# Performance work log

Hardware: AMD Instinct MI355X
Metric: run time of the kernel (lower is better)

The kernel has to match this reference:

```python
import jax, jax.numpy as jnp
import numpy as np

NUM_HEADS = 16
DIM = 1024

def setup_inputs() -> dict:
    key = jax.random.key(0)
    ks = jax.random.split(key, 12)
    B, N, T, C = 4, 4096, 77, DIM
    s = 1.0 / np.sqrt(C)
    return {
        "hidden_states": jax.random.normal(ks[0], (B, N, C), jnp.float32),
        "encoder_hidden_states": jax.random.normal(ks[1], (B, T, C), jnp.float32),
        "attention_mask": jnp.zeros((B, N, T), jnp.float32),
        "Wq": jax.random.normal(ks[2], (C, C), jnp.float32) * s,
        "bq": jnp.zeros((C,), jnp.float32),
        "Wk": jax.random.normal(ks[3], (C, C), jnp.float32) * s,
        "bk": jnp.zeros((C,), jnp.float32),
        "Wv": jax.random.normal(ks[4], (C, C), jnp.float32) * s,
        "bv": jnp.zeros((C,), jnp.float32),
        "Wo": jax.random.normal(ks[5], (C, C), jnp.float32) * s,
        "bo": jnp.zeros((C,), jnp.float32),
    }

def reference(hidden_states, encoder_hidden_states, attention_mask,
              Wq, bq, Wk, bk, Wv, bv, Wo, bo):
    B, N, C = hidden_states.shape
    T = encoder_hidden_states.shape[1]
    H = NUM_HEADS
    D = C // H
    # QKV projections (torch Linear: x @ W.T + b)
    q = (hidden_states @ Wq.T + bq).reshape(B, N, H, D).transpose(0, 2, 1, 3)   # bhnd
    k = (encoder_hidden_states @ Wk.T + bk).reshape(B, T, H, D).transpose(0, 2, 1, 3)  # bhtd
    v = (encoder_hidden_states @ Wv.T + bv).reshape(B, T, H, D).transpose(0, 2, 1, 3)  # bhtd
    scale = 1.0 / jnp.sqrt(jnp.asarray(D, q.dtype))
    # scores [B,H,N,T]; additive mask broadcast over heads
    scores = jnp.einsum('bhnd,bhtd->bhnt', q, k) * scale + attention_mask[:, None, :, :]
    attn = jax.nn.softmax(scores, axis=-1)
    out = jnp.einsum('bhnt,bhtd->bhnd', attn, v)
    out = out.transpose(0, 2, 1, 3).reshape(B, N, C)
    return out @ Wo.T + bo
```

## Files before the change

### kernel.cpp

```cpp
#include <hip/hip_runtime.h>
#include <cstdint>

typedef __bf16 bf16x8 __attribute__((ext_vector_type(8)));
typedef float f32x4 __attribute__((ext_vector_type(4)));
typedef unsigned short u16;
typedef unsigned int u32;

__device__ __forceinline__ u16 f2bf(float f) {
    u32 u = __builtin_bit_cast(u32, f);
    u += 0x7fffu + ((u >> 16) & 1u);
    return (u16)(u >> 16);
}

__device__ __forceinline__ void gl_lds16(const u16* g, u16* l) {
    __builtin_amdgcn_global_load_lds(
        (const __attribute__((address_space(1))) void*)g,
        (__attribute__((address_space(3))) void*)l,
        16, 0, 0);
}

__device__ __forceinline__ f32x4 mfma16(bf16x8 a, bf16x8 b, f32x4 c) {
    return __builtin_amdgcn_mfma_f32_16x16x32_bf16(a, b, c, 0, 0, 0);
}

__global__ void cvt_pad(const float* __restrict__ src, u16* __restrict__ dst,
                        int srcn, int totn) {
    int i = (blockIdx.x * 256 + threadIdx.x) * 4;
    if (i >= totn) return;
    float4 v = make_float4(0.f, 0.f, 0.f, 0.f);
    if (i < srcn) v = *(const float4*)&src[i];
    ushort4 o;
    o.x = f2bf(v.x); o.y = f2bf(v.y); o.z = f2bf(v.z); o.w = f2bf(v.w);
    *(ushort4*)&dst[i] = o;
}

struct CvtArgs {
    const float* s[5];
    u16* d[5];
    int srcn[5];
    int totn[5];
};

__global__ void cvt_multi(CvtArgs a) {
    const int seg = blockIdx.y;
    int i = (blockIdx.x * 256 + threadIdx.x) * 4;
    if (i >= a.totn[seg]) return;
    float4 v = make_float4(0.f, 0.f, 0.f, 0.f);
    if (i < a.srcn[seg]) v = *(const float4*)&a.s[seg][i];
    ushort4 o;
    o.x = f2bf(v.x); o.y = f2bf(v.y); o.z = f2bf(v.z); o.w = f2bf(v.w);
    *(ushort4*)&a.d[seg][i] = o;
}

__device__ __forceinline__ void store_out(u16* C, long idx, float v) { C[idx] = f2bf(v); }
__device__ __forceinline__ void store_out(float* C, long idx, float v) { C[idx] = v; }

template <typename OutT>
__global__ __launch_bounds__(512, 2) void gemm8p(
    const u16* __restrict__ A, const u16* __restrict__ W,
    const float* __restrict__ bias, OutT* __restrict__ C,
    int M, int N, int K) {
    __shared__ __align__(16) u16 As[2][256 * 64];
    __shared__ __align__(16) u16 Bs[2][256 * 64];

    const int tid = threadIdx.x;
    const int wid = tid >> 6, l = tid & 63;
    const int wr = wid >> 2, wc = wid & 3;
    const int l15 = l & 15, lg = l >> 4;

    const int lin = blockIdx.y * gridDim.x + blockIdx.x;
    const int cpx = (gridDim.x * gridDim.y) >> 3;
    const int swz = (lin & 7) * cpx + (lin >> 3);
    const long tn = swz % gridDim.x;
    const long tm = swz / gridDim.x;

    const u16* Ab = A + tm * 256 * (long)K;
    const u16* Bb = W + tn * 256 * (long)K;

    const int srow = tid >> 3;
    const int schunk = (tid & 7) ^ (srow & 7);
    const long srcoff = (long)srow * K + schunk * 8;

    const int rxor = l15 & 7;
    const int rdo0 = ((0 * 4 + lg) ^ rxor) * 8;
    const int rdo1 = ((1 * 4 + lg) ^ rxor) * 8;

    const int NT = K >> 6;

#define STAGE_A(bufi, q_, t_)                                                 \
    gl_lds16(Ab + (long)(q_)*64 * K + srcoff + (long)(t_)*64,                 \
             &As[bufi][(q_)*4096 + tid * 8])
#define STAGE_B(bufi, q_, t_)                                                 \
    gl_lds16(Bb + (long)(q_)*64 * K + srcoff + (long)(t_)*64,                 \
             &Bs[bufi][(q_)*4096 + tid * 8])

    f32x4 acc[8][4] = {};

#pragma unroll
    for (int q = 0; q < 4; ++q) { STAGE_A(0, q, 0); STAGE_B(0, q, 0); }
#pragma unroll
    for (int q = 0; q < 4; ++q) STAGE_B(1, q, 1);
    STAGE_A(1, 0, 1); STAGE_A(1, 2, 1);
    asm volatile("s_waitcnt vmcnt(6)" ::: "memory");
    __builtin_amdgcn_sched_barrier(0);
    __builtin_amdgcn_s_barrier();

    const int arow = wr * 128 + l15;
    const int brow = wc * 64 + l15;

    for (int t = 0; t < NT; ++t) {
        const int c = t & 1;
        const u16* __restrict__ Ap = &As[c][0];
        const u16* __restrict__ Bp = &Bs[c][0];
        const bool s1 = (t + 1) < NT;
        const bool s2 = (t + 2) < NT;
        bf16x8 b[4][2];

        {
            bf16x8 a[2][2];
#pragma unroll
            for (int mi = 0; mi < 2; ++mi) {
                a[mi][0] = *(const bf16x8*)&Ap[(arow + mi * 16) * 64 + rdo0];
                a[mi][1] = *(const bf16x8*)&Ap[(arow + mi * 16) * 64 + rdo1];
            }
#pragma unroll
            for (int nf = 0; nf < 4; ++nf) {
                b[nf][0] = *(const bf16x8*)&Bp[(brow + nf * 16) * 64 + rdo0];
                b[nf][1] = *(const bf16x8*)&Bp[(brow + nf * 16) * 64 + rdo1];
            }
            if (s1) STAGE_A(c ^ 1, 1, t + 1);
            __builtin_amdgcn_s_barrier();
            asm volatile("s_waitcnt lgkmcnt(0)" ::: "memory");
            __builtin_amdgcn_sched_barrier(0);
            __builtin_amdgcn_s_setprio(1);
#pragma unroll
            for (int mi = 0; mi < 2; ++mi)
#pragma unroll
                for (int nf = 0; nf < 4; ++nf) {
                    acc[mi][nf] = mfma16(a[mi][0], b[nf][0], acc[mi][nf]);
                    acc[mi][nf] = mfma16(a[mi][1], b[nf][1], acc[mi][nf]);
                }
            __builtin_amdgcn_s_setprio(0);
            __builtin_amdgcn_s_barrier();
        }
        {
            bf16x8 a[2][2];
#pragma unroll
            for (int mi = 0; mi < 2; ++mi) {
                a[mi][0] = *(const bf16x8*)&Ap[(arow + (mi + 2) * 16) * 64 + rdo0];
                a[mi][1] = *(const bf16x8*)&Ap[(arow + (mi + 2) * 16) * 64 + rdo1];
            }
            if (s1) STAGE_A(c ^ 1, 3, t + 1);
            if (s2) { STAGE_B(c, 0, t + 2); STAGE_B(c, 1, t + 2); }
            __builtin_amdgcn_s_barrier();
            asm volatile("s_waitcnt lgkmcnt(0)" ::: "memory");
            __builtin_amdgcn_sched_barrier(0);
            __builtin_amdgcn_s_setprio(1);
#pragma unroll
            for (int mi = 0; mi < 2; ++mi)
#pragma unroll
                for (int nf = 0; nf < 4; ++nf) {
                    acc[mi + 2][nf] = mfma16(a[mi][0], b[nf][0], acc[mi + 2][nf]);
                    acc[mi + 2][nf] = mfma16(a[mi][1], b[nf][1], acc[mi + 2][nf]);
                }
            __builtin_amdgcn_s_setprio(0);
            __builtin_amdgcn_s_barrier();
        }
        {
            bf16x8 a[2][2];
#pragma unroll
            for (int mi = 0; mi < 2; ++mi) {
                a[mi][0] = *(const bf16x8*)&Ap[(arow + (mi + 4) * 16) * 64 + rdo0];
                a[mi][1] = *(const bf16x8*)&Ap[(arow + (mi + 4) * 16) * 64 + rdo1];
            }
            if (s2) { STAGE_B(c, 2, t + 2); STAGE_B(c, 3, t + 2); STAGE_A(c, 0, t + 2); }
            __builtin_amdgcn_s_barrier();
            asm volatile("s_waitcnt lgkmcnt(0)" ::: "memory");
            __builtin_amdgcn_sched_barrier(0);
            __builtin_amdgcn_s_setprio(1);
#pragma unroll
            for (int mi = 0; mi < 2; ++mi)
#pragma unroll
                for (int nf = 0; nf < 4; ++nf) {
                    acc[mi + 4][nf] = mfma16(a[mi][0], b[nf][0], acc[mi + 4][nf]);
                    acc[mi + 4][nf] = mfma16(a[mi][1], b[nf][1], acc[mi + 4][nf]);
                }
            __builtin_amdgcn_s_setprio(0);
            __builtin_amdgcn_s_barrier();
        }
        {
            bf16x8 a[2][2];
#pragma unroll
            for (int mi = 0; mi < 2; ++mi) {
                a[mi][0] = *(const bf16x8*)&Ap[(arow + (mi + 6) * 16) * 64 + rdo0];
                a[mi][1] = *(const bf16x8*)&Ap[(arow + (mi + 6) * 16) * 64 + rdo1];
            }
            if (s2) STAGE_A(c, 2, t + 2);
            __builtin_amdgcn_s_barrier();
            asm volatile("s_waitcnt lgkmcnt(0)" ::: "memory");
            __builtin_amdgcn_sched_barrier(0);
            __builtin_amdgcn_s_setprio(1);
#pragma unroll
            for (int mi = 0; mi < 2; ++mi)
#pragma unroll
                for (int nf = 0; nf < 4; ++nf) {
                    acc[mi + 6][nf] = mfma16(a[mi][0], b[nf][0], acc[mi + 6][nf]);
                    acc[mi + 6][nf] = mfma16(a[mi][1], b[nf][1], acc[mi + 6][nf]);
                }
            __builtin_amdgcn_s_setprio(0);
            if (s2)
                asm volatile("s_waitcnt vmcnt(6)" ::: "memory");
            else
                asm volatile("s_waitcnt vmcnt(0)" ::: "memory");
            __builtin_amdgcn_sched_barrier(0);
            __builtin_amdgcn_s_barrier();
        }
    }
#undef STAGE_A
#undef STAGE_B

    const long row0 = tm * 256 + wr * 128;
    const long col0 = tn * 256 + wc * 64;
    float bv[4];
#pragma unroll
    for (int nf = 0; nf < 4; ++nf) bv[nf] = bias[col0 + nf * 16 + l15];
#pragma unroll
    for (int mf = 0; mf < 8; ++mf)
#pragma unroll
        for (int nf = 0; nf < 4; ++nf)
#pragma unroll
            for (int r = 0; r < 4; ++r) {
                const long row = row0 + mf * 16 + lg * 4 + r;
                const long col = col0 + nf * 16 + l15;
                store_out(C, row * N + col, acc[mf][nf][r] + bv[nf]);
            }
}

__device__ __forceinline__ void gemm128_body(
    const u16* __restrict__ A, const u16* __restrict__ W,
    const float* __restrict__ bias, u16* __restrict__ C,
    int N, int K) {
    __shared__ u16 As[128 * 64];
    __shared__ u16 Bs[128 * 64];
    const int tid = threadIdx.x;
    const int w = tid >> 6, l = tid & 63;
    const int wr = w >> 1, wc = w & 1;
    const int l15 = l & 15, lg = l >> 4;
    const long tm = blockIdx.y, tn = blockIdx.x;
    const u16* Ab = A + tm * 128 * (long)K;
    const u16* Bb = W + tn * 128 * (long)K;

    f32x4 acc[4][4] = {};

    for (int k0 = 0; k0 < K; k0 += 64) {
#pragma unroll
        for (int t = 0; t < 4; ++t) {
            int i = t * 256 + tid;
            int row = i >> 3, cc = i & 7;
            gl_lds16(Ab + (long)row * K + k0 + cc * 8, &As[i * 8]);
            gl_lds16(Bb + (long)row * K + k0 + cc * 8, &Bs[i * 8]);
        }
        __syncthreads();
#pragma unroll
        for (int kk = 0; kk < 64; kk += 32) {
            bf16x8 a[4], b[4];
#pragma unroll
            for (int m = 0; m < 4; ++m)
                a[m] = *(const bf16x8*)&As[(wr * 64 + m * 16 + l15) * 64 + kk + lg * 8];
#pragma unroll
            for (int n = 0; n < 4; ++n)
                b[n] = *(const bf16x8*)&Bs[(wc * 64 + n * 16 + l15) * 64 + kk + lg * 8];
#pragma unroll
            for (int m = 0; m < 4; ++m)
#pragma unroll
                for (int n = 0; n < 4; ++n)
                    acc[m][n] = mfma16(a[m], b[n], acc[m][n]);
        }
        __syncthreads();
    }

    const long row0 = tm * 128 + wr * 64;
    const long col0 = tn * 128 + wc * 64;
#pragma unroll
    for (int m = 0; m < 4; ++m)
#pragma unroll
        for (int n = 0; n < 4; ++n)
#pragma unroll
            for (int r = 0; r < 4; ++r) {
                const long row = row0 + m * 16 + lg * 4 + r;
                const long col = col0 + n * 16 + l15;
                C[row * N + col] = f2bf(acc[m][n][r] + bias[col]);
            }
}

__global__ __launch_bounds__(256) void gemm_kv(
    const u16* __restrict__ A,
    const u16* __restrict__ Wk, const float* __restrict__ bk, u16* __restrict__ Ko,
    const u16* __restrict__ Wv, const float* __restrict__ bv, u16* __restrict__ Vo,
    int N, int K) {
    const bool isv = blockIdx.z != 0;
    gemm128_body(A, isv ? Wv : Wk, isv ? bv : bk, isv ? Vo : Ko, N, K);
}

__global__ __launch_bounds__(256) void attn_fused(
    const u16* __restrict__ Q,
    const u16* __restrict__ Kb,
    const u16* __restrict__ Vb,
    const float* __restrict__ mask,
    u16* __restrict__ Ao) {
    __shared__ u16 Ks[96 * 64];
    __shared__ u16 Vt[64 * 96];
    __shared__ u16 Ps[128 * 96];

    const int b = blockIdx.z, h = blockIdx.y, nt = blockIdx.x;
    const int tid = threadIdx.x;
    const int w = tid >> 6, l = tid & 63;
    const int l15 = l & 15, lg = l >> 4;

    for (int c = tid; c < 768; c += 256) {
        const int t = c >> 3, dc = c & 7;
        union { uint4 u; u16 s[8]; } kv, vv;
        kv.u = make_uint4(0, 0, 0, 0);
        vv.u = make_uint4(0, 0, 0, 0);
        if (t < 77) {
            const long base = ((long)(b * 77 + t)) * 1024 + h * 64 + dc * 8;
            kv.u = *(const uint4*)&Kb[base];
            vv.u = *(const uint4*)&Vb[base];
        }
        *(uint4*)&Ks[t * 64 + dc * 8] = kv.u;
#pragma unroll
        for (int j = 0; j < 8; ++j) Vt[(dc * 8 + j) * 96 + t] = vv.s[j];
    }
    __syncthreads();

    f32x4 acc[2][6] = {};
    const long qrow0 = (long)b * 4096 + nt * 128 + w * 32;
#pragma unroll
    for (int kk = 0; kk < 64; kk += 32) {
        bf16x8 a[2], kf[6];
#pragma unroll
        for (int m = 0; m < 2; ++m)
            a[m] = *(const bf16x8*)&Q[(qrow0 + m * 16 + l15) * 1024 + h * 64 + kk + lg * 8];
#pragma unroll
        for (int n = 0; n < 6; ++n)
            kf[n] = *(const bf16x8*)&Ks[(n * 16 + l15) * 64 + kk + lg * 8];
#pragma unroll
        for (int m = 0; m < 2; ++m)
#pragma unroll
            for (int n = 0; n < 6; ++n)
                acc[m][n] = mfma16(a[m], kf[n], acc[m][n]);
    }

    const float* mbase = mask + ((long)b * 4096 + nt * 128 + w * 32) * 77;
#pragma unroll
    for (int m = 0; m < 2; ++m) {
#pragma unroll
        for (int r = 0; r < 4; ++r) {
            const int row = m * 16 + lg * 4 + r;
            float vals[6];
            float rmax = -3e38f;
#pragma unroll
            for (int n = 0; n < 6; ++n) {
                const int col = n * 16 + l15;
                float v = -3e38f;
                if (col < 77) v = acc[m][n][r] * 0.125f + mbase[row * 77 + col];
                vals[n] = v;
                rmax = fmaxf(rmax, v);
            }
#pragma unroll
            for (int off = 1; off < 16; off <<= 1)
                rmax = fmaxf(rmax, __shfl_xor(rmax, off, 64));
            float s = 0.f;
#pragma unroll
            for (int n = 0; n < 6; ++n) {
                float e = (vals[n] > -1e37f) ? __expf(vals[n] - rmax) : 0.f;
                vals[n] = e;
                s += e;
            }
#pragma unroll
            for (int off = 1; off < 16; off <<= 1)
                s += __shfl_xor(s, off, 64);
            const float inv = 1.f / s;
#pragma unroll
            for (int n = 0; n < 6; ++n)
                Ps[(w * 32 + row) * 96 + n * 16 + l15] = f2bf(vals[n] * inv);
        }
    }
    __syncthreads();

    f32x4 o[2][4] = {};
#pragma unroll
    for (int kt = 0; kt < 96; kt += 32) {
        bf16x8 a[2], vf[4];
#pragma unroll
        for (int m = 0; m < 2; ++m)
            a[m] = *(const bf16x8*)&Ps[(w * 32 + m * 16 + l15) * 96 + kt + lg * 8];
#pragma unroll
        for (int n = 0; n < 4; ++n)
            vf[n] = *(const bf16x8*)&Vt[(n * 16 + l15) * 96 + kt + lg * 8];
#pragma unroll
        for (int m = 0; m < 2; ++m)
#pragma unroll
            for (int n = 0; n < 4; ++n)
                o[m][n] = mfma16(a[m], vf[n], o[m][n]);
    }

#pragma unroll
    for (int m = 0; m < 2; ++m)
#pragma unroll
        for (int n = 0; n < 4; ++n)
#pragma unroll
            for (int r = 0; r < 4; ++r) {
                const long row = (long)b * 4096 + nt * 128 + w * 32 + m * 16 + lg * 4 + r;
                const int col = h * 64 + n * 16 + l15;
                Ao[row * 1024 + col] = f2bf(o[m][n][r]);
            }
}

extern "C" void kernel_launch(void* const* d_in, const int* in_sizes, int n_in,
                              void* d_out, int out_size, void* d_ws, size_t ws_size,
                              hipStream_t stream) {
    const float* hidden = (const float*)d_in[0];
    const float* enc = (const float*)d_in[1];
    const float* mask = (const float*)d_in[2];
    const float* Wq = (const float*)d_in[3];
    const float* bq = (const float*)d_in[4];
    const float* Wk = (const float*)d_in[5];
    const float* bk = (const float*)d_in[6];
    const float* Wv = (const float*)d_in[7];
    const float* bv = (const float*)d_in[8];
    const float* Wo = (const float*)d_in[9];
    const float* bo = (const float*)d_in[10];
    float* out = (float*)d_out;

    char* ws = (char*)d_ws;
    u16* hiddenB = (u16*)(ws);
    u16* Qb = (u16*)(ws + 33554432L);
    u16* AoB = (u16*)(ws + 2 * 33554432L);
    u16* WqB = (u16*)(ws + 3 * 33554432L);
    u16* WkB = WqB + 1048576;
    u16* WvB = WkB + 1048576;
    u16* WoB = WvB + 1048576;
    u16* encB = WoB + 1048576;
    u16* Kbuf = encB + 393216;
    u16* Vbuf = Kbuf + 393216;

    cvt_pad<<<dim3(16384), 256, 0, stream>>>(hidden, hiddenB, 16777216, 16777216);
    CvtArgs ca;
    ca.s[0] = Wq;  ca.d[0] = WqB; ca.srcn[0] = 1048576; ca.totn[0] = 1048576;
    ca.s[1] = Wk;  ca.d[1] = WkB; ca.srcn[1] = 1048576; ca.totn[1] = 1048576;
    ca.s[2] = Wv;  ca.d[2] = WvB; ca.srcn[2] = 1048576; ca.totn[2] = 1048576;
    ca.s[3] = Wo;  ca.d[3] = WoB; ca.srcn[3] = 1048576; ca.totn[3] = 1048576;
    ca.s[4] = enc; ca.d[4] = encB; ca.srcn[4] = 315392; ca.totn[4] = 393216;
    cvt_multi<<<dim3(1024, 5), 256, 0, stream>>>(ca);

    gemm8p<u16><<<dim3(4, 64), 512, 0, stream>>>(hiddenB, WqB, bq, Qb, 16384, 1024, 1024);
    gemm_kv<<<dim3(8, 3, 2), 256, 0, stream>>>(encB, WkB, bk, Kbuf, WvB, bv, Vbuf, 1024, 1024);

    attn_fused<<<dim3(32, 16, 4), 256, 0, stream>>>(Qb, Kbuf, Vbuf, mask, AoB);

    gemm8p<float><<<dim3(4, 64), 512, 0, stream>>>(AoB, WoB, bo, out, 16384, 1024, 1024);
}
```

Baseline: 163.3 us.

## Store intermediates in a blocked tile layout and reorder attention grid by head

Q, K, V and the attention output now live in a blocked layout: 16-column chunks, with four rows of 16 elements packed into one contiguous 64-element tile. The Q-projection epilogue, the KV GEMM epilogue, the attention loads and stores, and the output GEMM's A-staging all use this layout. The aim is to make each 16-byte fragment load and store in attention and the GEMM epilogues touch contiguous memory instead of rows strided by 1024 elements. The attention grid is also reordered so heads vary fastest, which may improve reuse of Q tiles in L2. The risk is that the index arithmetic becomes more complex and the GEMM A-operand staging becomes less sequential.

New measurement: 166.7 us. +2.1%, slower.

```diff
diff --git a/kernel.cpp b/kernel.cpp
--- a/kernel.cpp
+++ b/kernel.cpp
@@ -22,6 +22,7 @@
 __device__ __forceinline__ f32x4 mfma16(bf16x8 a, bf16x8 b, f32x4 c) {
     return __builtin_amdgcn_mfma_f32_16x16x32_bf16(a, b, c, 0, 0, 0);
 }
+
 
 __global__ void cvt_pad(const float* __restrict__ src, u16* __restrict__ dst,
                         int srcn, int totn) {
@@ -55,7 +56,7 @@
 __device__ __forceinline__ void store_out(u16* C, long idx, float v) { C[idx] = f2bf(v); }
 __device__ __forceinline__ void store_out(float* C, long idx, float v) { C[idx] = v; }
 
-template <typename OutT>
+template <typename OutT, bool BA, bool BC>
 __global__ __launch_bounds__(512, 2) void gemm8p(
     const u16* __restrict__ A, const u16* __restrict__ W,
     const float* __restrict__ bias, OutT* __restrict__ C,
@@ -74,12 +75,22 @@
     const long tn = swz % gridDim.x;
     const long tm = swz / gridDim.x;
 
-    const u16* Ab = A + tm * 256 * (long)K;
-    const u16* Bb = W + tn * 256 * (long)K;
-
     const int srow = tid >> 3;
     const int schunk = (tid & 7) ^ (srow & 7);
-    const long srcoff = (long)srow * K + schunk * 8;
+
+    long aBase, aQ, aT;
+    if (BA) {
+        const long rq = tm * 256 + srow;
+        aBase = ((long)(schunk >> 1) * (M >> 2) + (rq >> 2)) * 64 +
+                (srow & 3) * 16 + (schunk & 1) * 8;
+        aQ = 1024;
+        aT = 64L * M;
+    } else {
+        aBase = (tm * 256 + srow) * (long)K + schunk * 8;
+        aQ = 64L * K;
+        aT = 64;
+    }
+    const long bBase = (tn * 256 + srow) * (long)K + schunk * 8;
 
     const int rxor = l15 & 7;
     const int rdo0 = ((0 * 4 + lg) ^ rxor) * 8;
@@ -88,10 +99,9 @@
     const int NT = K >> 6;
 
 #define STAGE_A(bufi, q_, t_)                                                 \
-    gl_lds16(Ab + (long)(q_)*64 * K + srcoff + (long)(t_)*64,                 \
-             &As[bufi][(q_)*4096 + tid * 8])
+    gl_lds16(A + aBase + (q_)*aQ + (long)(t_)*aT, &As[bufi][(q_)*4096 + tid * 8])
 #define STAGE_B(bufi, q_, t_)                                                 \
-    gl_lds16(Bb + (long)(q_)*64 * K + srcoff + (long)(t_)*64,                 \
+    gl_lds16(W + bBase + (long)(q_)*64 * K + (long)(t_)*64,                   \
              &Bs[bufi][(q_)*4096 + tid * 8])
 
     f32x4 acc[8][4] = {};
@@ -224,16 +234,32 @@
     float bv[4];
 #pragma unroll
     for (int nf = 0; nf < 4; ++nf) bv[nf] = bias[col0 + nf * 16 + l15];
-#pragma unroll
-    for (int mf = 0; mf < 8; ++mf)
-#pragma unroll
-        for (int nf = 0; nf < 4; ++nf)
-#pragma unroll
-            for (int r = 0; r < 4; ++r) {
-                const long row = row0 + mf * 16 + lg * 4 + r;
-                const long col = col0 + nf * 16 + l15;
-                store_out(C, row * N + col, acc[mf][nf][r] + bv[nf]);
-            }
+    if (BC) {
+        const long ct0 = col0 >> 4;
+        const long rb = row0 >> 2;
+#pragma unroll
+        for (int mf = 0; mf < 8; ++mf)
+#pragma unroll
+            for (int nf = 0; nf < 4; ++nf)
+#pragma unroll
+                for (int r = 0; r < 4; ++r) {
+                    const long idx =
+                        ((ct0 + nf) * (long)(M >> 2) + rb + mf * 4 + lg) * 64 +
+                        r * 16 + l15;
+                    store_out(C, idx, acc[mf][nf][r] + bv[nf]);
+                }
+    } else {
+#pragma unroll
+        for (int mf = 0; mf < 8; ++mf)
+#pragma unroll
+            for (int nf = 0; nf < 4; ++nf)
+#pragma unroll
+                for (int r = 0; r < 4; ++r) {
+                    const long row = row0 + mf * 16 + lg * 4 + r;
+                    const long col = col0 + nf * 16 + l15;
+                    store_out(C, row * N + col, acc[mf][nf][r] + bv[nf]);
+                }
+    }
 }
 
 __device__ __forceinline__ void gemm128_body(
@@ -287,9 +313,9 @@
         for (int n = 0; n < 4; ++n)
 #pragma unroll
             for (int r = 0; r < 4; ++r) {
-                const long row = row0 + m * 16 + lg * 4 + r;
-                const long col = col0 + n * 16 + l15;
-                C[row * N + col] = f2bf(acc[m][n][r] + bias[col]);
+                const long idx = (((col0 >> 4) + n) * 96L + (row0 >> 2) + m * 4 + lg) * 64 +
+                                 r * 16 + l15;
+                C[idx] = f2bf(acc[m][n][r] + bias[col0 + n * 16 + l15]);
             }
 }
 
@@ -312,7 +338,7 @@
     __shared__ u16 Vt[64 * 96];
     __shared__ u16 Ps[128 * 96];
 
-    const int b = blockIdx.z, h = blockIdx.y, nt = blockIdx.x;
+    const int h = blockIdx.x, nt = blockIdx.y, b = blockIdx.z;
     const int tid = threadIdx.x;
     const int w = tid >> 6, l = tid & 63;
     const int l15 = l & 15, lg = l >> 4;
@@ -323,7 +349,9 @@
         kv.u = make_uint4(0, 0, 0, 0);
         vv.u = make_uint4(0, 0, 0, 0);
         if (t < 77) {
-            const long base = ((long)(b * 77 + t)) * 1024 + h * 64 + dc * 8;
+            const int row = b * 77 + t;
+            const long base = ((long)(h * 4 + (dc >> 1)) * 96 + (row >> 2)) * 64 +
+                              (row & 3) * 16 + (dc & 1) * 8;
             kv.u = *(const uint4*)&Kb[base];
             vv.u = *(const uint4*)&Vb[base];
         }
@@ -334,13 +362,15 @@
     __syncthreads();
 
     f32x4 acc[2][6] = {};
-    const long qrow0 = (long)b * 4096 + nt * 128 + w * 32;
+    const int rq = b * 4096 + nt * 128 + w * 32;
 #pragma unroll
     for (int kk = 0; kk < 64; kk += 32) {
         bf16x8 a[2], kf[6];
 #pragma unroll
         for (int m = 0; m < 2; ++m)
-            a[m] = *(const bf16x8*)&Q[(qrow0 + m * 16 + l15) * 1024 + h * 64 + kk + lg * 8];
+            a[m] = *(const bf16x8*)&Q[((long)(h * 4 + (kk >> 4) + (lg >> 1)) * 4096 +
+                                       (rq >> 2) + m * 4 + (l15 >> 2)) * 64 +
+                                      (l15 & 3) * 16 + (lg & 1) * 8];
 #pragma unroll
         for (int n = 0; n < 6; ++n)
             kf[n] = *(const bf16x8*)&Ks[(n * 16 + l15) * 64 + kk + lg * 8];
@@ -411,9 +441,10 @@
         for (int n = 0; n < 4; ++n)
 #pragma unroll
             for (int r = 0; r < 4; ++r) {
-                const long row = (long)b * 4096 + nt * 128 + w * 32 + m * 16 + lg * 4 + r;
-                const int col = h * 64 + n * 16 + l15;
-                Ao[row * 1024 + col] = f2bf(o[m][n][r]);
+                const long idx = ((long)(h * 4 + n) * 4096 +
+                                  b * 1024 + nt * 32 + w * 8 + m * 4 + lg) * 64 +
+                                 r * 16 + l15;
+                Ao[idx] = f2bf(o[m][n][r]);
             }
 }
 
@@ -454,10 +485,12 @@
     ca.s[4] = enc; ca.d[4] = encB; ca.srcn[4] = 315392; ca.totn[4] = 393216;
     cvt_multi<<<dim3(1024, 5), 256, 0, stream>>>(ca);
 
-    gemm8p<u16><<<dim3(4, 64), 512, 0, stream>>>(hiddenB, WqB, bq, Qb, 16384, 1024, 1024);
+    gemm8p<u16, false, true><<<dim3(4, 64), 512, 0, stream>>>(
+        hiddenB, WqB, bq, Qb, 16384, 1024, 1024);
     gemm_kv<<<dim3(8, 3, 2), 256, 0, stream>>>(encB, WkB, bk, Kbuf, WvB, bv, Vbuf, 1024, 1024);
 
-    attn_fused<<<dim3(32, 16, 4), 256, 0, stream>>>(Qb, Kbuf, Vbuf, mask, AoB);
-
-    gemm8p<float><<<dim3(4, 64), 512, 0, stream>>>(AoB, WoB, bo, out, 16384, 1024, 1024);
-}
+    attn_fused<<<dim3(16, 32, 4), 256, 0, stream>>>(Qb, Kbuf, Vbuf, mask, AoB);
+
+    gemm8p<float, true, false><<<dim3(4, 64), 512, 0, stream>>>(
+        AoB, WoB, bo, out, 16384, 1024, 1024);
+}
```
